# Optimization experiments

Measured on AMD Instinct MI355X. Metric: run time of the kernel, lower is better.

The kernel has to match this reference:

```python
import jax, jax.numpy as jnp
import numpy as np

D_IN = 1024
D_OUT = 1024


def setup_inputs() -> dict:
    key = jax.random.key(0)
    kx, kq, kk, kv = jax.random.split(key, 4)
    s = 1.0 / np.sqrt(D_IN)
    x = jax.random.normal(kx, (2, 4096, D_IN), dtype=jnp.float32)
    # nn.Linear weights: shape [d_out, d_in], y = x @ W.T (no bias)
    W_query = jax.random.normal(kq, (D_OUT, D_IN), dtype=jnp.float32) * s
    W_key = jax.random.normal(kk, (D_OUT, D_IN), dtype=jnp.float32) * s
    W_value = jax.random.normal(kv, (D_OUT, D_IN), dtype=jnp.float32) * s
    return {"x": x, "W_query": W_query, "W_key": W_key, "W_value": W_value}


def reference(x, W_query, W_key, W_value):
    # QKV projections: [b, n, d_in] @ [d_in, d_out]
    q = jnp.einsum('bnd,od->bno', x, W_query)
    k = jnp.einsum('bnd,od->bno', x, W_key)
    v = jnp.einsum('bnd,od->bno', x, W_value)
    d_k = k.shape[-1]
    scores = jnp.einsum('bqo,bko->bqk', q, k) / jnp.sqrt(jnp.asarray(d_k, x.dtype))
    # NOTE: source applies no causal mask despite the class name
    attn = jax.nn.softmax(scores, axis=-1)
    return jnp.einsum('bqk,bko->bqo', attn, v)
```

## Files before the change

### kernel.cpp

```cpp
#include <hip/hip_runtime.h>
#include <hip/hip_bf16.h>
#include <hip/hip_fp16.h>
#include <stdint.h>

typedef __bf16 bf16_t;
typedef __bf16 bf16x8 __attribute__((ext_vector_type(8)));
typedef float f32x4 __attribute__((ext_vector_type(4)));

typedef __attribute__((address_space(1))) void gv_t;
typedef __attribute__((address_space(3))) void lv_t;

__device__ inline unsigned short f2bf_bits(float f) {
  uint32_t u = __float_as_uint(f);
  u += 0x7FFFu + ((u >> 16) & 1u);
  return (unsigned short)(u >> 16);
}
__device__ inline bf16_t f2bf(float f) {
  unsigned short h = f2bf_bits(f);
  return __builtin_bit_cast(bf16_t, h);
}

__device__ inline void storeC(float* p, float v) { *p = v; }
__device__ inline void storeC(bf16_t* p, float v) { *p = f2bf(v); }
__device__ inline void storeC(__half* p, float v) { *p = __float2half(v); }

__device__ inline void xcd_remap(int64_t& bm, int64_t& bn) {
  const int gx  = gridDim.x;
  const int h   = blockIdx.x + gx * blockIdx.y;
  const int gpx = gx >> 3;
  const int xcd = h & 7;
  const int s   = h >> 3;
  bm = xcd * gpx + (s % gpx);
  bn = s / gpx;
}

__global__ __launch_bounds__(256)
void convert_all(const float* __restrict__ x, const float* __restrict__ wq,
                 const float* __restrict__ wk, const float* __restrict__ wv,
                 bf16_t* __restrict__ xb, bf16_t* __restrict__ wqkb,
                 bf16_t* __restrict__ wvb)
{
  const int64_t NX = 8192LL * 1024, NW = 1024LL * 1024;
  const int64_t total4 = (NX + 3 * NW) >> 2;
  for (int64_t i = (int64_t)blockIdx.x * blockDim.x + threadIdx.x; i < total4;
       i += (int64_t)gridDim.x * blockDim.x) {
    int64_t e = i << 2;
    const float* src; bf16_t* dst; int64_t off;
    if (e < NX)               { src = x;  dst = xb;         off = e; }
    else if (e < NX + NW)     { src = wq; dst = wqkb;       off = e - NX; }
    else if (e < NX + 2 * NW) { src = wk; dst = wqkb + NW;  off = e - NX - NW; }
    else                      { src = wv; dst = wvb;        off = e - NX - 2 * NW; }
    float4 f = *(const float4*)(src + off);
    uint32_t lo = ((uint32_t)f2bf_bits(f.y) << 16) | f2bf_bits(f.x);
    uint32_t hi = ((uint32_t)f2bf_bits(f.w) << 16) | f2bf_bits(f.z);
    *(uint2*)(dst + off) = make_uint2(lo, hi);
  }
}

template <typename OUT_T>
__global__ __launch_bounds__(256)
void gemm_bt(const bf16_t* __restrict__ A, const bf16_t* __restrict__ B,
             OUT_T* __restrict__ C, int K, int lda, int ldb, int ldc,
             int64_t b_batch_stride, int bm_per_batch)
{
  __shared__ bf16_t As[2][128 * 32];
  __shared__ bf16_t Bs[2][128 * 32];
  const int tid  = threadIdx.x;
  const int wid  = tid >> 6;
  const int lane = tid & 63;
  const int wm = wid >> 1, wn = wid & 1;
  const int64_t bm = blockIdx.x;
  const int64_t bn = blockIdx.y;

  const bf16_t* Bb = B + (bm / bm_per_batch) * b_batch_stride;

  const int c0row = (wid * 2 + 0) * 16 + (lane >> 2);
  const int c1row = (wid * 2 + 1) * 16 + (lane >> 2);
  const int scol  = (lane & 3) * 8;

  const bf16_t* Ar0 = A  + (bm * 128 + c0row) * lda + scol;
  const bf16_t* Ar1 = A  + (bm * 128 + c1row) * lda + scol;
  const bf16_t* Br0 = Bb + (bn * 128 + c0row) * ldb + scol;
  const bf16_t* Br1 = Bb + (bn * 128 + c1row) * ldb + scol;

  const int ad0 = (wid * 2 + 0) * 512;
  const int ad1 = (wid * 2 + 1) * 512;

  const int frow = lane & 15;
  const int fk   = (lane >> 4) * 8;
  const int aoff = (wm * 64 + frow) * 32 + fk;
  const int boff = (wn * 64 + frow) * 32 + fk;

  f32x4 acc[4][4];
  #pragma unroll
  for (int m = 0; m < 4; m++)
    #pragma unroll
    for (int n = 0; n < 4; n++) acc[m][n] = f32x4{0.f, 0.f, 0.f, 0.f};

  auto stage = [&](int buf, int k0) {
    __builtin_amdgcn_global_load_lds((const gv_t*)(Ar0 + k0),
                                     (lv_t*)(&As[buf][ad0]), 16, 0, 0);
    __builtin_amdgcn_global_load_lds((const gv_t*)(Ar1 + k0),
                                     (lv_t*)(&As[buf][ad1]), 16, 0, 0);
    __builtin_amdgcn_global_load_lds((const gv_t*)(Br0 + k0),
                                     (lv_t*)(&Bs[buf][ad0]), 16, 0, 0);
    __builtin_amdgcn_global_load_lds((const gv_t*)(Br1 + k0),
                                     (lv_t*)(&Bs[buf][ad1]), 16, 0, 0);
  };

  stage(0, 0);
  __syncthreads();
  int cur = 0;
  for (int k0 = 0; k0 < K; k0 += 32) {
    if (k0 + 32 < K) stage(cur ^ 1, k0 + 32);

    bf16x8 af[4], bfr[4];
    #pragma unroll
    for (int m = 0; m < 4; m++)
      af[m] = *(const bf16x8*)(&As[cur][aoff + m * 16 * 32]);
    #pragma unroll
    for (int n = 0; n < 4; n++)
      bfr[n] = *(const bf16x8*)(&Bs[cur][boff + n * 16 * 32]);
    #pragma unroll
    for (int m = 0; m < 4; m++)
      #pragma unroll
      for (int n = 0; n < 4; n++)
        acc[m][n] = __builtin_amdgcn_mfma_f32_16x16x32_bf16(af[m], bfr[n],
                                                            acc[m][n], 0, 0, 0);
    __syncthreads();
    cur ^= 1;
  }

  const int crow = (lane >> 4) * 4;
  const int ccol = lane & 15;
  #pragma unroll
  for (int m = 0; m < 4; m++)
    #pragma unroll
    for (int n = 0; n < 4; n++)
      #pragma unroll
      for (int j = 0; j < 4; j++) {
        int64_t row = bm * 128 + wm * 64 + m * 16 + crow + j;
        int64_t col = bn * 128 + wn * 64 + n * 16 + ccol;
        storeC(&C[row * ldc + col], acc[m][n][j]);
      }
}

template <typename OUT_T, typename OUT2_T>
__global__ __launch_bounds__(512, 2)
void gemm256(const bf16_t* __restrict__ A, const bf16_t* __restrict__ B,
             OUT_T* __restrict__ C0, OUT2_T* __restrict__ C1,
             int K, int lda, int ldb, int ldc,
             int64_t b_batch_stride, int bm_per_batch,
             int64_t za_off, int64_t zb_off)
{
  __shared__ bf16_t As[2][256][64];
  __shared__ bf16_t Bs[2][256][64];

  const int tid  = threadIdx.x;
  const int wid  = tid >> 6;
  const int lane = tid & 63;
  const int wm = wid >> 2;
  const int wn = wid & 3;
  int64_t bm, bn;
  xcd_remap(bm, bn);
  const int z = blockIdx.z;

  const bf16_t* Ap = A + (int64_t)z * za_off;
  const bf16_t* Bp = B + (bm / bm_per_batch) * b_batch_stride
                       + (int64_t)z * zb_off;

  const int srow  = tid >> 3;
  const int sslot = (tid & 7) ^ (srow & 7);
  const int64_t lda64 = lda, ldb64 = ldb;
  const bf16_t* Ag = Ap + (bm * 256 + srow) * lda64 + sslot * 8;
  const bf16_t* Bg = Bp + (bn * 256 + srow) * ldb64 + sslot * 8;

  auto stageA = [&](int buf, int t, int q) {
    const bf16_t* src = Ag + (int64_t)(q * 64) * lda64 + t * 64;
    char* dst = (char*)&As[buf][0][0] + (q * 64 + wid * 8) * 128;
    __builtin_amdgcn_global_load_lds((const gv_t*)src, (lv_t*)dst, 16, 0, 0);
  };
  auto stageB = [&](int buf, int t, int q) {
    const bf16_t* src = Bg + (int64_t)(q * 64) * ldb64 + t * 64;
    char* dst = (char*)&Bs[buf][0][0] + (q * 64 + wid * 8) * 128;
    __builtin_amdgcn_global_load_lds((const gv_t*)src, (lv_t*)dst, 16, 0, 0);
  };

  const int frow   = lane & 15;
  const int fcol16 = lane >> 4;
  const int xorv   = (lane & 7) << 4;
  const int ck0 = (fcol16 * 16) ^ xorv;
  const int ck1 = (64 + fcol16 * 16) ^ xorv;
  const int arowb = (wm * 128 + frow) * 128;
  const int browb = (wn * 64  + frow) * 128;

  f32x4 acc[8][4];
  #pragma unroll
  for (int m = 0; m < 8; m++)
    #pragma unroll
    for (int n = 0; n < 4; n++) acc[m][n] = f32x4{0.f, 0.f, 0.f, 0.f};

  const int NT = K >> 6;

  #pragma unroll
  for (int q = 0; q < 4; q++) stageA(0, 0, q);
  #pragma unroll
  for (int q = 0; q < 4; q++) stageB(0, 0, q);
  asm volatile("s_waitcnt vmcnt(0)" ::: "memory");
  __builtin_amdgcn_s_barrier();
  __builtin_amdgcn_sched_barrier(0);

  bf16x8 a[8][2], bb[4][2];

  for (int g = 0; g < NT; ++g) {
    const int buf = g & 1;
    const char* lA = (const char*)&As[buf][0][0];
    const char* lB = (const char*)&Bs[buf][0][0];

    #pragma unroll
    for (int m = 0; m < 8; m++)
      a[m][0] = *(const bf16x8*)(lA + arowb + m * 2048 + ck0);
    #pragma unroll
    for (int n = 0; n < 4; n++)
      bb[n][0] = *(const bf16x8*)(lB + browb + n * 2048 + ck0);
    #pragma unroll
    for (int m = 0; m < 8; m++)
      a[m][1] = *(const bf16x8*)(lA + arowb + m * 2048 + ck1);
    #pragma unroll
    for (int n = 0; n < 4; n++)
      bb[n][1] = *(const bf16x8*)(lB + browb + n * 2048 + ck1);

    if (g + 1 < NT) {
      #pragma unroll
      for (int q = 0; q < 4; q++) stageA(buf ^ 1, g + 1, q);
      #pragma unroll
      for (int q = 0; q < 4; q++) stageB(buf ^ 1, g + 1, q);
    }

    __builtin_amdgcn_s_setprio(1);
    #pragma unroll
    for (int k = 0; k < 2; k++)
      #pragma unroll
      for (int m = 0; m < 8; m++)
        #pragma unroll
        for (int n = 0; n < 4; n++)
          acc[m][n] = __builtin_amdgcn_mfma_f32_16x16x32_bf16(
              a[m][k], bb[n][k], acc[m][n], 0, 0, 0);
    __builtin_amdgcn_s_setprio(0);

    asm volatile("s_waitcnt vmcnt(0)" ::: "memory");
    __builtin_amdgcn_s_barrier();
    __builtin_amdgcn_sched_barrier(0);
  }

  const int crow = (lane >> 4) * 4;
  const int ccol = lane & 15;
  if (z == 0) {
    #pragma unroll
    for (int m = 0; m < 8; m++)
      #pragma unroll
      for (int n = 0; n < 4; n++)
        #pragma unroll
        for (int j = 0; j < 4; j++) {
          int64_t row = bm * 256 + wm * 128 + m * 16 + crow + j;
          int64_t col = bn * 256 + wn * 64 + n * 16 + ccol;
          storeC(&C0[row * (int64_t)ldc + col], acc[m][n][j]);
        }
  } else {
    #pragma unroll
    for (int m = 0; m < 8; m++)
      #pragma unroll
      for (int n = 0; n < 4; n++)
        #pragma unroll
        for (int j = 0; j < 4; j++) {
          int64_t row = bm * 256 + wm * 128 + m * 16 + crow + j;
          int64_t col = bn * 256 + wn * 64 + n * 16 + ccol;
          storeC(&C1[row * (int64_t)ldc + col], acc[m][n][j]);
        }
  }
}

template <typename OUT_T, typename OUT2_T>
__global__ __launch_bounds__(256, 2)
void gemm128(const bf16_t* __restrict__ A, const bf16_t* __restrict__ B,
             OUT_T* __restrict__ C0, OUT2_T* __restrict__ C1,
             int K, int lda, int ldb, int ldc,
             int64_t b_batch_stride, int bm_per_batch,
             int64_t za_off, int64_t zb_off)
{
  __shared__ bf16_t As[2][128][64];
  __shared__ bf16_t Bs[2][128][64];

  const int tid  = threadIdx.x;
  const int wid  = tid >> 6;
  const int lane = tid & 63;
  const int wm = wid >> 1;
  const int wn = wid & 1;
  int64_t bm, bn;
  xcd_remap(bm, bn);
  const int z = blockIdx.z;

  const bf16_t* Ap = A + (int64_t)z * za_off;
  const bf16_t* Bp = B + (bm / bm_per_batch) * b_batch_stride
                       + (int64_t)z * zb_off;

  const int srow  = tid >> 3;
  const int sslot = (tid & 7) ^ (srow & 7);
  const int64_t lda64 = lda, ldb64 = ldb;
  const bf16_t* Ag = Ap + (bm * 128 + srow) * lda64 + sslot * 8;
  const bf16_t* Bg = Bp + (bn * 128 + srow) * ldb64 + sslot * 8;

  auto stageA = [&](int buf, int t, int q) {
    const bf16_t* src = Ag + (int64_t)(q * 32) * lda64 + t * 64;
    char* dst = (char*)&As[buf][0][0] + (q * 32 + wid * 8) * 128;
    __builtin_amdgcn_global_load_lds((const gv_t*)src, (lv_t*)dst, 16, 0, 0);
  };
  auto stageB = [&](int buf, int t, int q) {
    const bf16_t* src = Bg + (int64_t)(q * 32) * ldb64 + t * 64;
    char* dst = (char*)&Bs[buf][0][0] + (q * 32 + wid * 8) * 128;
    __builtin_amdgcn_global_load_lds((const gv_t*)src, (lv_t*)dst, 16, 0, 0);
  };

  const int frow   = lane & 15;
  const int fcol16 = lane >> 4;
  const int xorv   = (lane & 7) << 4;
  const int ck0 = (fcol16 * 16) ^ xorv;
  const int ck1 = (64 + fcol16 * 16) ^ xorv;
  const int arowb = (wm * 64 + frow) * 128;
  const int browb = (wn * 64 + frow) * 128;

  f32x4 acc[4][4];
  #pragma unroll
  for (int m = 0; m < 4; m++)
    #pragma unroll
    for (int n = 0; n < 4; n++) acc[m][n] = f32x4{0.f, 0.f, 0.f, 0.f};

  const int NT = K >> 6;

  stageA(0, 0, 0); stageA(0, 0, 1); stageA(0, 0, 2); stageA(0, 0, 3);
  stageB(0, 0, 0); stageB(0, 0, 1); stageB(0, 0, 2); stageB(0, 0, 3);
  asm volatile("s_waitcnt vmcnt(0)" ::: "memory");
  __builtin_amdgcn_s_barrier();
  __builtin_amdgcn_sched_barrier(0);

  bf16x8 a[4][2], bb[4][2];

  for (int g = 0; g < NT; ++g) {
    const int buf = g & 1;
    const char* lA = (const char*)&As[buf][0][0];
    const char* lB = (const char*)&Bs[buf][0][0];

    #pragma unroll
    for (int m = 0; m < 4; m++)
      a[m][0] = *(const bf16x8*)(lA + arowb + m * 2048 + ck0);
    #pragma unroll
    for (int n = 0; n < 4; n++)
      bb[n][0] = *(const bf16x8*)(lB + browb + n * 2048 + ck0);
    #pragma unroll
    for (int m = 0; m < 4; m++)
      a[m][1] = *(const bf16x8*)(lA + arowb + m * 2048 + ck1);
    #pragma unroll
    for (int n = 0; n < 4; n++)
      bb[n][1] = *(const bf16x8*)(lB + browb + n * 2048 + ck1);

    if (g + 1 < NT) {
      stageA(buf ^ 1, g + 1, 0); stageA(buf ^ 1, g + 1, 1);
      stageA(buf ^ 1, g + 1, 2); stageA(buf ^ 1, g + 1, 3);
      stageB(buf ^ 1, g + 1, 0); stageB(buf ^ 1, g + 1, 1);
      stageB(buf ^ 1, g + 1, 2); stageB(buf ^ 1, g + 1, 3);
    }

    __builtin_amdgcn_s_setprio(1);
    #pragma unroll
    for (int k = 0; k < 2; k++)
      #pragma unroll
      for (int m = 0; m < 4; m++)
        #pragma unroll
        for (int n = 0; n < 4; n++)
          acc[m][n] = __builtin_amdgcn_mfma_f32_16x16x32_bf16(
              a[m][k], bb[n][k], acc[m][n], 0, 0, 0);
    __builtin_amdgcn_s_setprio(0);

    asm volatile("s_waitcnt vmcnt(0)" ::: "memory");
    __builtin_amdgcn_s_barrier();
    __builtin_amdgcn_sched_barrier(0);
  }

  const int crow = (lane >> 4) * 4;
  const int ccol = lane & 15;
  if (z == 0) {
    #pragma unroll
    for (int m = 0; m < 4; m++)
      #pragma unroll
      for (int n = 0; n < 4; n++)
        #pragma unroll
        for (int j = 0; j < 4; j++) {
          int64_t row = bm * 128 + wm * 64 + m * 16 + crow + j;
          int64_t col = bn * 128 + wn * 64 + n * 16 + ccol;
          storeC(&C0[row * (int64_t)ldc + col], acc[m][n][j]);
        }
  } else {
    #pragma unroll
    for (int m = 0; m < 4; m++)
      #pragma unroll
      for (int n = 0; n < 4; n++)
        #pragma unroll
        for (int j = 0; j < 4; j++) {
          int64_t row = bm * 128 + wm * 64 + m * 16 + crow + j;
          int64_t col = bn * 128 + wn * 64 + n * 16 + ccol;
          storeC(&C1[row * (int64_t)ldc + col], acc[m][n][j]);
        }
  }
}

__global__ __launch_bounds__(256)
void softmax_rows(__half* __restrict__ SP)
{
  const int64_t row = blockIdx.x;
  __half* s = SP + row * 4096;
  bf16_t* p = (bf16_t*)s;
  const int tid = threadIdx.x;
  const float scale = 0.03125f;

  float v[16];
  float vmax = -3.4e38f;
  #pragma unroll
  for (int i = 0; i < 4; i++) {
    uint2 raw = *(const uint2*)(s + i * 1024 + tid * 4);
    __half2 h01 = __builtin_bit_cast(__half2, raw.x);
    __half2 h23 = __builtin_bit_cast(__half2, raw.y);
    float2 f01 = __half22float2(h01);
    float2 f23 = __half22float2(h23);
    v[i * 4 + 0] = f01.x * scale;
    v[i * 4 + 1] = f01.y * scale;
    v[i * 4 + 2] = f23.x * scale;
    v[i * 4 + 3] = f23.y * scale;
    vmax = fmaxf(vmax, fmaxf(fmaxf(v[i*4+0], v[i*4+1]),
                             fmaxf(v[i*4+2], v[i*4+3])));
  }
  #pragma unroll
  for (int o = 32; o > 0; o >>= 1) vmax = fmaxf(vmax, __shfl_xor(vmax, o));
  __shared__ float redm[4];
  __shared__ float reds[4];
  if ((tid & 63) == 0) redm[tid >> 6] = vmax;
  __syncthreads();
  vmax = fmaxf(fmaxf(redm[0], redm[1]), fmaxf(redm[2], redm[3]));

  float lsum = 0.f;
  #pragma unroll
  for (int i = 0; i < 16; i++) {
    v[i] = __expf(v[i] - vmax);
    lsum += v[i];
  }
  #pragma unroll
  for (int o = 32; o > 0; o >>= 1) lsum += __shfl_xor(lsum, o);
  if ((tid & 63) == 0) reds[tid >> 6] = lsum;
  __syncthreads();
  lsum = (reds[0] + reds[1]) + (reds[2] + reds[3]);
  const float inv = 1.0f / lsum;

  #pragma unroll
  for (int i = 0; i < 4; i++) {
    uint32_t lo = ((uint32_t)f2bf_bits(v[i*4+1] * inv) << 16) | f2bf_bits(v[i*4+0] * inv);
    uint32_t hi = ((uint32_t)f2bf_bits(v[i*4+3] * inv) << 16) | f2bf_bits(v[i*4+2] * inv);
    *(uint2*)(p + i * 1024 + tid * 4) = make_uint2(lo, hi);
  }
}

extern "C" void kernel_launch(void* const* d_in, const int* in_sizes, int n_in,
                              void* d_out, int out_size, void* d_ws, size_t ws_size,
                              hipStream_t stream) {
  const float* x  = (const float*)d_in[0];
  const float* wq = (const float*)d_in[1];
  const float* wk = (const float*)d_in[2];
  const float* wv = (const float*)d_in[3];
  float* out = (float*)d_out;

  char* ws = (char*)d_ws;
  bf16_t* xb   = (bf16_t*)ws;
  bf16_t* wqkb = (bf16_t*)(ws + (16LL << 20));
  bf16_t* wvb  = (bf16_t*)(ws + (20LL << 20));
  __half* S    = (__half*)ws;
  bf16_t* qk   = (bf16_t*)(ws + (64LL << 20));
  bf16_t* vt   = (bf16_t*)(ws + (96LL << 20));

  const int NO_BATCH = 1 << 30;

  convert_all<<<2048, 256, 0, stream>>>(x, wq, wk, wv, xb, wqkb, wvb);

  gemm256<bf16_t, bf16_t><<<dim3(32, 8, 1), 512, 0, stream>>>(
      xb, wqkb, qk, qk, 1024, 1024, 1024, 2048, 0, NO_BATCH, 0, 0);

  gemm_bt<bf16_t><<<dim3(8, 64), 256, 0, stream>>>(
      wvb, xb, vt, 1024, 1024, 1024, 8192, 0, NO_BATCH);

  gemm256<__half, __half><<<dim3(32, 16, 1), 512, 0, stream>>>(
      qk, qk + 1024, S, S, 1024, 2048, 2048, 4096, 4096LL * 2048, 16, 0, 0);

  softmax_rows<<<8192, 256, 0, stream>>>(S);

  gemm128<float, float><<<dim3(64, 8, 1), 256, 0, stream>>>(
      (const bf16_t*)S, vt, out, out, 4096, 4096, 8192, 1024,
      4096, 32, 0, 0);
}
```

Before: 217.1 us.

## Fuse exp and row-sum into QK^T GEMM epilogue, defer normalization to PV

Computes exp(scale*score) directly in the score GEMM epilogue, writes bf16 exponentials and per-warp partial row sums, then reduces the sums in a tiny kernel and applies 1/sum in the PV GEMM epilogue. This removes the separate softmax pass over the full score matrix. It drops max-subtraction, so very large scores could overflow. It also swaps the simple V-transpose GEMM for the tuned 128-tile GEMM.

```diff
diff --git a/kernel.cpp b/kernel.cpp
--- a/kernel.cpp
+++ b/kernel.cpp
@@ -1,6 +1,5 @@
 #include <hip/hip_runtime.h>
 #include <hip/hip_bf16.h>
-#include <hip/hip_fp16.h>
 #include <stdint.h>
 
 typedef __bf16 bf16_t;
@@ -22,7 +21,6 @@
 
 __device__ inline void storeC(float* p, float v) { *p = v; }
 __device__ inline void storeC(bf16_t* p, float v) { *p = f2bf(v); }
-__device__ inline void storeC(__half* p, float v) { *p = __float2half(v); }
 
 __device__ inline void xcd_remap(int64_t& bm, int64_t& bn) {
   const int gx  = gridDim.x;
@@ -57,101 +55,14 @@
   }
 }
 
-template <typename OUT_T>
-__global__ __launch_bounds__(256)
-void gemm_bt(const bf16_t* __restrict__ A, const bf16_t* __restrict__ B,
-             OUT_T* __restrict__ C, int K, int lda, int ldb, int ldc,
-             int64_t b_batch_stride, int bm_per_batch)
-{
-  __shared__ bf16_t As[2][128 * 32];
-  __shared__ bf16_t Bs[2][128 * 32];
-  const int tid  = threadIdx.x;
-  const int wid  = tid >> 6;
-  const int lane = tid & 63;
-  const int wm = wid >> 1, wn = wid & 1;
-  const int64_t bm = blockIdx.x;
-  const int64_t bn = blockIdx.y;
-
-  const bf16_t* Bb = B + (bm / bm_per_batch) * b_batch_stride;
-
-  const int c0row = (wid * 2 + 0) * 16 + (lane >> 2);
-  const int c1row = (wid * 2 + 1) * 16 + (lane >> 2);
-  const int scol  = (lane & 3) * 8;
-
-  const bf16_t* Ar0 = A  + (bm * 128 + c0row) * lda + scol;
-  const bf16_t* Ar1 = A  + (bm * 128 + c1row) * lda + scol;
-  const bf16_t* Br0 = Bb + (bn * 128 + c0row) * ldb + scol;
-  const bf16_t* Br1 = Bb + (bn * 128 + c1row) * ldb + scol;
-
-  const int ad0 = (wid * 2 + 0) * 512;
-  const int ad1 = (wid * 2 + 1) * 512;
-
-  const int frow = lane & 15;
-  const int fk   = (lane >> 4) * 8;
-  const int aoff = (wm * 64 + frow) * 32 + fk;
-  const int boff = (wn * 64 + frow) * 32 + fk;
-
-  f32x4 acc[4][4];
-  #pragma unroll
-  for (int m = 0; m < 4; m++)
-    #pragma unroll
-    for (int n = 0; n < 4; n++) acc[m][n] = f32x4{0.f, 0.f, 0.f, 0.f};
-
-  auto stage = [&](int buf, int k0) {
-    __builtin_amdgcn_global_load_lds((const gv_t*)(Ar0 + k0),
-                                     (lv_t*)(&As[buf][ad0]), 16, 0, 0);
-    __builtin_amdgcn_global_load_lds((const gv_t*)(Ar1 + k0),
-                                     (lv_t*)(&As[buf][ad1]), 16, 0, 0);
-    __builtin_amdgcn_global_load_lds((const gv_t*)(Br0 + k0),
-                                     (lv_t*)(&Bs[buf][ad0]), 16, 0, 0);
-    __builtin_amdgcn_global_load_lds((const gv_t*)(Br1 + k0),
-                                     (lv_t*)(&Bs[buf][ad1]), 16, 0, 0);
-  };
-
-  stage(0, 0);
-  __syncthreads();
-  int cur = 0;
-  for (int k0 = 0; k0 < K; k0 += 32) {
-    if (k0 + 32 < K) stage(cur ^ 1, k0 + 32);
-
-    bf16x8 af[4], bfr[4];
-    #pragma unroll
-    for (int m = 0; m < 4; m++)
-      af[m] = *(const bf16x8*)(&As[cur][aoff + m * 16 * 32]);
-    #pragma unroll
-    for (int n = 0; n < 4; n++)
-      bfr[n] = *(const bf16x8*)(&Bs[cur][boff + n * 16 * 32]);
-    #pragma unroll
-    for (int m = 0; m < 4; m++)
-      #pragma unroll
-      for (int n = 0; n < 4; n++)
-        acc[m][n] = __builtin_amdgcn_mfma_f32_16x16x32_bf16(af[m], bfr[n],
-                                                            acc[m][n], 0, 0, 0);
-    __syncthreads();
-    cur ^= 1;
-  }
-
-  const int crow = (lane >> 4) * 4;
-  const int ccol = lane & 15;
-  #pragma unroll
-  for (int m = 0; m < 4; m++)
-    #pragma unroll
-    for (int n = 0; n < 4; n++)
-      #pragma unroll
-      for (int j = 0; j < 4; j++) {
-        int64_t row = bm * 128 + wm * 64 + m * 16 + crow + j;
-        int64_t col = bn * 128 + wn * 64 + n * 16 + ccol;
-        storeC(&C[row * ldc + col], acc[m][n][j]);
-      }
-}
-
-template <typename OUT_T, typename OUT2_T>
+template <bool EXPSUM, typename OUT_T, typename OUT2_T>
 __global__ __launch_bounds__(512, 2)
 void gemm256(const bf16_t* __restrict__ A, const bf16_t* __restrict__ B,
              OUT_T* __restrict__ C0, OUT2_T* __restrict__ C1,
              int K, int lda, int ldb, int ldc,
              int64_t b_batch_stride, int bm_per_batch,
-             int64_t za_off, int64_t zb_off)
+             int64_t za_off, int64_t zb_off,
+             float* __restrict__ sums_part, float escale)
 {
   __shared__ bf16_t As[2][256][64];
   __shared__ bf16_t Bs[2][256][64];
@@ -255,6 +166,17 @@
 
   const int crow = (lane >> 4) * 4;
   const int ccol = lane & 15;
+
+  if (EXPSUM) {
+    #pragma unroll
+    for (int m = 0; m < 8; m++)
+      #pragma unroll
+      for (int n = 0; n < 4; n++)
+        #pragma unroll
+        for (int j = 0; j < 4; j++)
+          acc[m][n][j] = __expf(acc[m][n][j] * escale);
+  }
+
   if (z == 0) {
     #pragma unroll
     for (int m = 0; m < 8; m++)
@@ -278,15 +200,32 @@
           storeC(&C1[row * (int64_t)ldc + col], acc[m][n][j]);
         }
   }
-}
-
-template <typename OUT_T, typename OUT2_T>
+
+  if (EXPSUM) {
+    const int64_t widx = bn * 4 + wn;
+    #pragma unroll
+    for (int m = 0; m < 8; m++)
+      #pragma unroll
+      for (int j = 0; j < 4; j++) {
+        float rs = acc[m][0][j] + acc[m][1][j] + acc[m][2][j] + acc[m][3][j];
+        rs += __shfl_xor(rs, 1);
+        rs += __shfl_xor(rs, 2);
+        rs += __shfl_xor(rs, 4);
+        rs += __shfl_xor(rs, 8);
+        if (ccol == 0) {
+          int64_t row = bm * 256 + wm * 128 + m * 16 + crow + j;
+          sums_part[widx * 8192 + row] = rs;
+        }
+      }
+  }
+}
+
+template <bool NORM, typename OUT_T>
 __global__ __launch_bounds__(256, 2)
 void gemm128(const bf16_t* __restrict__ A, const bf16_t* __restrict__ B,
-             OUT_T* __restrict__ C0, OUT2_T* __restrict__ C1,
-             int K, int lda, int ldb, int ldc,
+             OUT_T* __restrict__ C0, int K, int lda, int ldb, int ldc,
              int64_t b_batch_stride, int bm_per_batch,
-             int64_t za_off, int64_t zb_off)
+             const float* __restrict__ sums)
 {
   __shared__ bf16_t As[2][128][64];
   __shared__ bf16_t Bs[2][128][64];
@@ -298,16 +237,13 @@
   const int wn = wid & 1;
   int64_t bm, bn;
   xcd_remap(bm, bn);
-  const int z = blockIdx.z;
-
-  const bf16_t* Ap = A + (int64_t)z * za_off;
-  const bf16_t* Bp = B + (bm / bm_per_batch) * b_batch_stride
-                       + (int64_t)z * zb_off;
+
+  const bf16_t* Bp = B + (bm / bm_per_batch) * b_batch_stride;
 
   const int srow  = tid >> 3;
   const int sslot = (tid & 7) ^ (srow & 7);
   const int64_t lda64 = lda, ldb64 = ldb;
-  const bf16_t* Ag = Ap + (bm * 128 + srow) * lda64 + sslot * 8;
+  const bf16_t* Ag = A  + (bm * 128 + srow) * lda64 + sslot * 8;
   const bf16_t* Bg = Bp + (bn * 128 + srow) * ldb64 + sslot * 8;
 
   auto stageA = [&](int buf, int t, int q) {
@@ -388,83 +324,39 @@
 
   const int crow = (lane >> 4) * 4;
   const int ccol = lane & 15;
-  if (z == 0) {
+
+  if (NORM) {
     #pragma unroll
     for (int m = 0; m < 4; m++)
       #pragma unroll
-      for (int n = 0; n < 4; n++)
-        #pragma unroll
-        for (int j = 0; j < 4; j++) {
-          int64_t row = bm * 128 + wm * 64 + m * 16 + crow + j;
-          int64_t col = bn * 128 + wn * 64 + n * 16 + ccol;
-          storeC(&C0[row * (int64_t)ldc + col], acc[m][n][j]);
-        }
-  } else {
-    #pragma unroll
-    for (int m = 0; m < 4; m++)
-      #pragma unroll
-      for (int n = 0; n < 4; n++)
-        #pragma unroll
-        for (int j = 0; j < 4; j++) {
-          int64_t row = bm * 128 + wm * 64 + m * 16 + crow + j;
-          int64_t col = bn * 128 + wn * 64 + n * 16 + ccol;
-          storeC(&C1[row * (int64_t)ldc + col], acc[m][n][j]);
-        }
-  }
+      for (int j = 0; j < 4; j++) {
+        int64_t row = bm * 128 + wm * 64 + m * 16 + crow + j;
+        float inv = 1.0f / sums[row];
+        #pragma unroll
+        for (int n = 0; n < 4; n++) acc[m][n][j] *= inv;
+      }
+  }
+
+  #pragma unroll
+  for (int m = 0; m < 4; m++)
+    #pragma unroll
+    for (int n = 0; n < 4; n++)
+      #pragma unroll
+      for (int j = 0; j < 4; j++) {
+        int64_t row = bm * 128 + wm * 64 + m * 16 + crow + j;
+        int64_t col = bn * 128 + wn * 64 + n * 16 + ccol;
+        storeC(&C0[row * (int64_t)ldc + col], acc[m][n][j]);
+      }
 }
 
 __global__ __launch_bounds__(256)
-void softmax_rows(__half* __restrict__ SP)
+void reduce_sums(const float* __restrict__ part, float* __restrict__ sums)
 {
-  const int64_t row = blockIdx.x;
-  __half* s = SP + row * 4096;
-  bf16_t* p = (bf16_t*)s;
-  const int tid = threadIdx.x;
-  const float scale = 0.03125f;
-
-  float v[16];
-  float vmax = -3.4e38f;
-  #pragma unroll
-  for (int i = 0; i < 4; i++) {
-    uint2 raw = *(const uint2*)(s + i * 1024 + tid * 4);
-    __half2 h01 = __builtin_bit_cast(__half2, raw.x);
-    __half2 h23 = __builtin_bit_cast(__half2, raw.y);
-    float2 f01 = __half22float2(h01);
-    float2 f23 = __half22float2(h23);
-    v[i * 4 + 0] = f01.x * scale;
-    v[i * 4 + 1] = f01.y * scale;
-    v[i * 4 + 2] = f23.x * scale;
-    v[i * 4 + 3] = f23.y * scale;
-    vmax = fmaxf(vmax, fmaxf(fmaxf(v[i*4+0], v[i*4+1]),
-                             fmaxf(v[i*4+2], v[i*4+3])));
-  }
-  #pragma unroll
-  for (int o = 32; o > 0; o >>= 1) vmax = fmaxf(vmax, __shfl_xor(vmax, o));
-  __shared__ float redm[4];
-  __shared__ float reds[4];
-  if ((tid & 63) == 0) redm[tid >> 6] = vmax;
-  __syncthreads();
-  vmax = fmaxf(fmaxf(redm[0], redm[1]), fmaxf(redm[2], redm[3]));
-
-  float lsum = 0.f;
-  #pragma unroll
-  for (int i = 0; i < 16; i++) {
-    v[i] = __expf(v[i] - vmax);
-    lsum += v[i];
-  }
-  #pragma unroll
-  for (int o = 32; o > 0; o >>= 1) lsum += __shfl_xor(lsum, o);
-  if ((tid & 63) == 0) reds[tid >> 6] = lsum;
-  __syncthreads();
-  lsum = (reds[0] + reds[1]) + (reds[2] + reds[3]);
-  const float inv = 1.0f / lsum;
-
-  #pragma unroll
-  for (int i = 0; i < 4; i++) {
-    uint32_t lo = ((uint32_t)f2bf_bits(v[i*4+1] * inv) << 16) | f2bf_bits(v[i*4+0] * inv);
-    uint32_t hi = ((uint32_t)f2bf_bits(v[i*4+3] * inv) << 16) | f2bf_bits(v[i*4+2] * inv);
-    *(uint2*)(p + i * 1024 + tid * 4) = make_uint2(lo, hi);
-  }
+  const int r = blockIdx.x * 256 + threadIdx.x;
+  float s = 0.f;
+  #pragma unroll
+  for (int i = 0; i < 64; i++) s += part[i * 8192 + r];
+  sums[r] = s;
 }
 
 extern "C" void kernel_launch(void* const* d_in, const int* in_sizes, int n_in,
@@ -480,26 +372,29 @@
   bf16_t* xb   = (bf16_t*)ws;
   bf16_t* wqkb = (bf16_t*)(ws + (16LL << 20));
   bf16_t* wvb  = (bf16_t*)(ws + (20LL << 20));
-  __half* S    = (__half*)ws;
+  bf16_t* E    = (bf16_t*)ws;
   bf16_t* qk   = (bf16_t*)(ws + (64LL << 20));
   bf16_t* vt   = (bf16_t*)(ws + (96LL << 20));
+  float* sums_part = (float*)(ws + (112LL << 20));
+  float* sums      = (float*)(ws + (114LL << 20));
 
   const int NO_BATCH = 1 << 30;
 
   convert_all<<<2048, 256, 0, stream>>>(x, wq, wk, wv, xb, wqkb, wvb);
 
-  gemm256<bf16_t, bf16_t><<<dim3(32, 8, 1), 512, 0, stream>>>(
-      xb, wqkb, qk, qk, 1024, 1024, 1024, 2048, 0, NO_BATCH, 0, 0);
-
-  gemm_bt<bf16_t><<<dim3(8, 64), 256, 0, stream>>>(
-      wvb, xb, vt, 1024, 1024, 1024, 8192, 0, NO_BATCH);
-
-  gemm256<__half, __half><<<dim3(32, 16, 1), 512, 0, stream>>>(
-      qk, qk + 1024, S, S, 1024, 2048, 2048, 4096, 4096LL * 2048, 16, 0, 0);
-
-  softmax_rows<<<8192, 256, 0, stream>>>(S);
-
-  gemm128<float, float><<<dim3(64, 8, 1), 256, 0, stream>>>(
-      (const bf16_t*)S, vt, out, out, 4096, 4096, 8192, 1024,
-      4096, 32, 0, 0);
-}
+  gemm256<false, bf16_t, bf16_t><<<dim3(32, 8, 1), 512, 0, stream>>>(
+      xb, wqkb, qk, qk, 1024, 1024, 1024, 2048, 0, NO_BATCH, 0, 0,
+      nullptr, 0.f);
+
+  gemm128<false, bf16_t><<<dim3(8, 64, 1), 256, 0, stream>>>(
+      wvb, xb, vt, 1024, 1024, 1024, 8192, 0, NO_BATCH, nullptr);
+
+  gemm256<true, bf16_t, bf16_t><<<dim3(32, 16, 1), 512, 0, stream>>>(
+      qk, qk + 1024, E, E, 1024, 2048, 2048, 4096, 4096LL * 2048, 16, 0, 0,
+      sums_part, 0.03125f);
+
+  reduce_sums<<<32, 256, 0, stream>>>(sums_part, sums);
+
+  gemm128<true, float><<<dim3(64, 8, 1), 256, 0, stream>>>(
+      E, vt, out, 4096, 4096, 8192, 1024, 4096, 32, sums);
+}
```

After: 222.5 us. 1.03x slower.
